# Optimization experiments

Hardware: AMD Instinct MI355X
Metric: run time of the kernel (lower is better)

The kernel has to match this reference:

```python
import jax, jax.numpy as jnp
import numpy as np

# irreps '32x0e + 32x1o + 16x2e': dims 32 (l=0), 96 (l=1, 32x3), 80 (l=2, 16x5) -> 208
MUL0, MUL1, MUL2 = 32, 32, 16
SC = 64  # scalar_channels
N_NODES, N_EDGES = 50000, 200000
FAN_IN = MUL0 * MUL0 + MUL1 * MUL1 + MUL2 * MUL2  # fully-connected path fan-in


def setup_inputs() -> dict:
    key = jax.random.key(0)
    ks = jax.random.split(key, 10)
    node_tensors = jax.random.normal(ks[0], (N_NODES, 208), dtype=jnp.float32)
    edge_index = jax.random.randint(ks[1], (2, N_EDGES), 0, N_NODES)
    # FullyConnectedTensorProduct path weights (mul1, mul2, mul_out)
    W0 = jax.random.normal(ks[2], (MUL0, MUL0, SC), dtype=jnp.float32)
    W1 = jax.random.normal(ks[3], (MUL1, MUL1, SC), dtype=jnp.float32)
    W2 = jax.random.normal(ks[4], (MUL2, MUL2, SC), dtype=jnp.float32)
    # MLP: Linear(64,32) -> SiLU -> Linear(32,1)
    A1 = jax.random.normal(ks[5], (SC, SC // 2), dtype=jnp.float32) / np.float32(np.sqrt(SC))
    b1 = jnp.zeros((SC // 2,), dtype=jnp.float32)
    A2 = jax.random.normal(ks[6], (SC // 2, 1), dtype=jnp.float32) / np.float32(np.sqrt(SC // 2))
    b2 = jnp.zeros((1,), dtype=jnp.float32)
    return {"node_tensors": node_tensors, "edge_index": edge_index,
            "W0": W0, "W1": W1, "W2": W2, "A1": A1, "b1": b1, "A2": A2, "b2": b2}


def _split_irreps(x):
    # x: [E, 208] -> scalars [E,32], vectors [E,32,3], rank-2 [E,16,5]
    s = x[:, :MUL0]
    v = x[:, MUL0:MUL0 + MUL1 * 3].reshape(-1, MUL1, 3)
    t = x[:, MUL0 + MUL1 * 3:].reshape(-1, MUL2, 5)
    return s, v, t


def reference(node_tensors, edge_index, W0, W1, W2, A1, b1, A2, b2):
    src, dst = edge_index[0], edge_index[1]
    x1 = node_tensors[src]  # [E, 208]
    x2 = node_tensors[dst]
    s1, v1, t1 = _split_irreps(x1)
    s2, v2, t2 = _split_irreps(x2)
    alpha = np.float32(1.0 / np.sqrt(FAN_IN))  # path normalization
    # l x l -> 0 Clebsch-Gordan: delta_{m1 m2} / sqrt(2l+1)
    e = alpha * (
        jnp.einsum('eu,ev,uvw->ew', s1, s2, W0)
        + jnp.einsum('eum,evm,uvw->ew', v1, v2, W1) / np.float32(np.sqrt(3.0))
        + jnp.einsum('eum,evm,uvw->ew', t1, t2, W2) / np.float32(np.sqrt(5.0))
    )  # [E, 64]
    h = jax.nn.silu(e @ A1 + b1)
    return (h @ A2 + b2)[:, 0]  # [E]
```

## Files before the change

### kernel.cpp

```cpp
#include <hip/hip_runtime.h>
#include <hip/hip_fp16.h>
#include <stdint.h>

#define N_EDGES 200000
#define N_NODES 50000
#define BM 32
#define NT 64

typedef _Float16 f16x8 __attribute__((ext_vector_type(8)));
typedef float f32x4 __attribute__((ext_vector_type(4)));

__global__ void prep_w(const float* __restrict__ W0, const float* __restrict__ W1,
                       const float* __restrict__ W2, uint16_t* __restrict__ wt) {
  int o = blockIdx.x * 256 + threadIdx.x;
  int T = o >> 11, r = o & 2047, w = r >> 5, kk = r & 31;
  int k = T * 32 + kk;
  const float AS = 1.0f / 48.0f;
  const float AV = AS * 0.57735026918962576f;
  const float AT = AS * 0.44721359549995794f;
  float val;
  if (k < 1024)      val = AS * W0[(k >> 5) * 2048 + (k & 31) * 64 + w];
  else if (k < 2048) { int k2 = k - 1024; val = AV * W1[(k2 >> 5) * 2048 + (k2 & 31) * 64 + w]; }
  else               { int k2 = k - 2048; val = AT * W2[(k2 >> 4) * 1024 + (k2 & 15) * 64 + w]; }
  __half h = __float2half(val);
  wt[o] = *reinterpret_cast<uint16_t*>(&h);
}

__global__ void prep_tables(const float* __restrict__ nt,
                            uint16_t* __restrict__ ta, uint16_t* __restrict__ tb) {
  long long o = (long long)blockIdx.x * 256 + threadIdx.x;
  if (o >= (long long)N_NODES * 296) return;
  int node = (int)(o / 296);
  int r = (int)(o - (long long)node * 296);
  const float* x = nt + (size_t)node * 208;
  float va = 0.f;
  if (r < 32) va = x[r];
  else if (r < 160) { int q = r - 32;  int u = q >> 2, m = q & 3;  if (m < 3) va = x[32 + u * 3 + m]; }
  else if (r < 288) { int q = r - 160; int u = q >> 3, m = q & 7;  if (m < 5) va = x[128 + u * 5 + m]; }
  __half ha = __float2half(va);
  ta[(size_t)node * 296 + r] = *reinterpret_cast<uint16_t*>(&ha);
  if (r < 216) {
    float vb = 0.f;
    if (r < 32) vb = x[r];
    else if (r < 128) { int q = r - 32;  int m = q >> 5, v = q & 31; vb = x[32 + v * 3 + m]; }
    else if (r < 208) { int q = r - 128; int m = q >> 4, v = q & 15; vb = x[128 + v * 5 + m]; }
    __half hb = __float2half(vb);
    tb[(size_t)node * 216 + r] = *reinterpret_cast<uint16_t*>(&hb);
  }
}

__device__ __forceinline__ void gload16(const void* g, void* l) {
  __builtin_amdgcn_global_load_lds(
      (const __attribute__((address_space(1))) void*)g,
      (__attribute__((address_space(3))) void*)l, 16, 0, 0);
}

#define LOADW(WRA, TEXPR)                                                       \
  { int Tc_ = (TEXPR);                                                          \
    _Pragma("unroll") for (int nf = 0; nf < 4; ++nf)                            \
      WRA[nf] = wtg4[Tc_ * 256 + nf * 64 + lo4]; }

#define MSTEPA(WRA, A)                                                          \
  _Pragma("unroll") for (int mf = 0; mf < 2; ++mf)                              \
  _Pragma("unroll") for (int nf = 0; nf < 4; ++nf)                              \
    acc[mf][nf] = __builtin_amdgcn_mfma_f32_16x16x32_f16(                       \
        (A)[mf], *(const f16x8*)&WRA[nf], acc[mf][nf], 0, 0, 0);

#define BUILD_S(T_, A)                                                          \
  _Pragma("unroll") for (int mf = 0; mf < 2; ++mf) {                            \
    __half s1v = *(const __half*)(x1b[mf] + 2 * (T_));                          \
    __half2 s1b2 = __half2half2(s1v);                                           \
    union { uint32_t u[4]; f16x8 v; } au_;                                      \
    _Pragma("unroll") for (int q = 0; q < 4; ++q) {                             \
      __half2 p = __hmul2(s1b2, ((const __half2*)&s2pk[mf])[q]);                \
      au_.u[q] = *(uint32_t*)&p;                                                \
    }                                                                           \
    (A)[mf] = au_.v;                                                            \
  }

#define BUILD_V(U_, A)                                                          \
  _Pragma("unroll") for (int mf = 0; mf < 2; ++mf) {                            \
    uint2 vv_ = *(const uint2*)(x1b[mf] + 64 + (U_) * 8);                       \
    __half2 h01_ = *(__half2*)&vv_.x;                                           \
    __half2 h2x_ = *(__half2*)&vv_.y;                                           \
    __half2 va0 = __half2half2(__low2half(h01_));                               \
    __half2 va1 = __half2half2(__high2half(h01_));                              \
    __half2 va2 = __half2half2(__low2half(h2x_));                               \
    union { uint32_t u[4]; f16x8 v; } au_;                                      \
    _Pragma("unroll") for (int q = 0; q < 4; ++q) {                             \
      __half2 p = __hmul2(va0, ((const __half2*)&v2pk[mf][0])[q]);              \
      p = __hfma2(va1, ((const __half2*)&v2pk[mf][1])[q], p);                   \
      p = __hfma2(va2, ((const __half2*)&v2pk[mf][2])[q], p);                   \
      au_.u[q] = *(uint32_t*)&p;                                                \
    }                                                                           \
    (A)[mf] = au_.v;                                                            \
  }

#define BUILD_T(TT_, A)                                                         \
  _Pragma("unroll") for (int mm = 0; mm < 2; ++mm) {                            \
    int u_ = (TT_) * 2 + (g >> 1);                                              \
    uint4 tv_ = *(const uint4*)(x1b[mm] + 320 + u_ * 16);                       \
    __half2 w01_ = *(__half2*)&tv_.x;                                           \
    __half2 w23_ = *(__half2*)&tv_.y;                                           \
    __half2 w4x_ = *(__half2*)&tv_.z;                                           \
    __half2 tb0 = __half2half2(__low2half(w01_));                               \
    __half2 tb1 = __half2half2(__high2half(w01_));                              \
    __half2 tb2 = __half2half2(__low2half(w23_));                               \
    __half2 tb3 = __half2half2(__high2half(w23_));                              \
    __half2 tb4 = __half2half2(__low2half(w4x_));                               \
    union { uint32_t u[4]; f16x8 v; } au_;                                      \
    _Pragma("unroll") for (int q = 0; q < 4; ++q) {                             \
      __half2 p = __hmul2(tb0, ((const __half2*)&t2pk[mm][0])[q]);              \
      p = __hfma2(tb1, ((const __half2*)&t2pk[mm][1])[q], p);                   \
      p = __hfma2(tb2, ((const __half2*)&t2pk[mm][2])[q], p);                   \
      p = __hfma2(tb3, ((const __half2*)&t2pk[mm][3])[q], p);                   \
      p = __hfma2(tb4, ((const __half2*)&t2pk[mm][4])[q], p);                   \
      au_.u[q] = *(uint32_t*)&p;                                                \
    }                                                                           \
    (A)[mm] = au_.v;                                                            \
  }

#define RING_S(WRA, P, T0) { f16x8 a[2]; BUILD_S((T0) + (P), a); MSTEPA(WRA, a); LOADW(WRA, (T0) + (P) + 4); }
#define RING_V(WRA, P, T0) { f16x8 a[2]; BUILD_V((T0) + (P) - 32, a); MSTEPA(WRA, a); LOADW(WRA, (T0) + (P) + 4); }
#define WRAPT(X) ((X) <= 71 ? (X) : (X) - 8)
#define RING_T(WRA, P, T0) { f16x8 a[2]; BUILD_T((T0) + (P) - 64, a); MSTEPA(WRA, a); LOADW(WRA, WRAPT((T0) + (P) + 4)); }

__global__ __launch_bounds__(NT) void edge_main(
    const uint16_t* __restrict__ ta, const uint16_t* __restrict__ tbl,
    const int* __restrict__ ei, const uint16_t* __restrict__ wt,
    const float* __restrict__ A1, const float* __restrict__ b1,
    const float* __restrict__ A2, const float* __restrict__ b2,
    float* __restrict__ out)
{
  __shared__ alignas(16) unsigned char smem[18944];
  const int tid = threadIdx.x;
  const int e0 = blockIdx.x * BM;

  {
    #pragma unroll
    for (int i = 0; i < 18; ++i) {
      unsigned idx = i * 64 + tid;
      unsigned row = idx / 37u;
      unsigned cj = idx - row * 37u;
      int e = e0 + (int)row;
      int src = ei[e];
      const char* gp = (const char*)ta + (size_t)src * 592 + cj * 16;
      gload16(gp, (void*)(smem + i * 1024));
    }
    if (tid < 32) {
      unsigned idx = 1152 + tid;
      unsigned row = idx / 37u;
      unsigned cj = idx - row * 37u;
      int e = e0 + (int)row;
      int src = ei[e];
      const char* gp = (const char*)ta + (size_t)src * 592 + cj * 16;
      gload16(gp, (void*)(smem + 18432));
    }
  }
  asm volatile("s_waitcnt vmcnt(0)" ::: "memory");

  const int lane = tid, c = lane & 15, g = lane >> 4;
  const int lo4 = c * 4 + g;

  const unsigned char* x1b[2];
  const unsigned char* tbp[2];
  #pragma unroll
  for (int mf = 0; mf < 2; ++mf) {
    int erow = mf * 16 + c;
    x1b[mf] = smem + (size_t)erow * 592;
    int e = e0 + erow;
    int dst = ei[N_EDGES + e];
    tbp[mf] = (const unsigned char*)tbl + (size_t)dst * 432;
  }

  f32x4 acc[2][4];
  #pragma unroll
  for (int mf = 0; mf < 2; ++mf)
    #pragma unroll
    for (int nf = 0; nf < 4; ++nf) acc[mf][nf] = (f32x4){0.f, 0.f, 0.f, 0.f};

  const uint4* wtg4 = (const uint4*)wt;
  uint4 wr0[4], wr1[4], wr2[4], wr3[4];

  {
    uint4 s2pk[2];
    #pragma unroll
    for (int mf = 0; mf < 2; ++mf) s2pk[mf] = *(const uint4*)(tbp[mf] + g * 16);
    LOADW(wr0, 0); LOADW(wr1, 1); LOADW(wr2, 2); LOADW(wr3, 3);
    for (int T = 0; T < 32; T += 4) {
      RING_S(wr0, 0, T); RING_S(wr1, 1, T); RING_S(wr2, 2, T); RING_S(wr3, 3, T);
    }
  }
  {
    uint4 v2pk[2][3];
    #pragma unroll
    for (int mf = 0; mf < 2; ++mf)
      #pragma unroll
      for (int m3 = 0; m3 < 3; ++m3)
        v2pk[mf][m3] = *(const uint4*)(tbp[mf] + 64 + m3 * 64 + g * 16);
    for (int T = 32; T < 64; T += 4) {
      RING_V(wr0, 0, T); RING_V(wr1, 1, T); RING_V(wr2, 2, T); RING_V(wr3, 3, T);
    }
  }
  {
    uint4 t2pk[2][5];
    #pragma unroll
    for (int mm = 0; mm < 2; ++mm)
      #pragma unroll
      for (int m5 = 0; m5 < 5; ++m5)
        t2pk[mm][m5] = *(const uint4*)(tbp[mm] + 256 + m5 * 32 + (g & 1) * 16);
    RING_T(wr0, 0, 64); RING_T(wr1, 1, 64); RING_T(wr2, 2, 64); RING_T(wr3, 3, 64);
    RING_T(wr0, 0, 68); RING_T(wr1, 1, 68); RING_T(wr2, 2, 68); RING_T(wr3, 3, 68);
  }

  float* ew = (float*)smem;
  #pragma unroll
  for (int mf = 0; mf < 2; ++mf)
    #pragma unroll
    for (int nf = 0; nf < 4; ++nf)
      #pragma unroll
      for (int rr = 0; rr < 4; ++rr)
        ew[(size_t)(mf * 16 + g * 4 + rr) * 68 + nf * 16 + c] = acc[mf][nf][rr];

  {
    int el = lane >> 1, jh = lane & 1;
    const float* er = ew + (size_t)el * 68;
    float hacc[16];
    #pragma unroll
    for (int j = 0; j < 16; ++j) hacc[j] = b1[jh * 16 + j];
    for (int w4 = 0; w4 < 16; ++w4) {
      float4 ea = *(const float4*)(er + w4 * 4);
      #pragma unroll
      for (int q2 = 0; q2 < 4; ++q2) {
        float ev = (&ea.x)[q2];
        int w = w4 * 4 + q2;
        float4 a0 = *(const float4*)(A1 + w * 32 + jh * 16);
        float4 a1 = *(const float4*)(A1 + w * 32 + jh * 16 + 4);
        float4 a2 = *(const float4*)(A1 + w * 32 + jh * 16 + 8);
        float4 a3 = *(const float4*)(A1 + w * 32 + jh * 16 + 12);
        hacc[0]  += ev * a0.x; hacc[1]  += ev * a0.y; hacc[2]  += ev * a0.z; hacc[3]  += ev * a0.w;
        hacc[4]  += ev * a1.x; hacc[5]  += ev * a1.y; hacc[6]  += ev * a1.z; hacc[7]  += ev * a1.w;
        hacc[8]  += ev * a2.x; hacc[9]  += ev * a2.y; hacc[10] += ev * a2.z; hacc[11] += ev * a2.w;
        hacc[12] += ev * a3.x; hacc[13] += ev * a3.y; hacc[14] += ev * a3.z; hacc[15] += ev * a3.w;
      }
    }
    float o = 0.f;
    #pragma unroll
    for (int j = 0; j < 16; ++j) {
      float z = hacc[j];
      o += (z / (1.f + __expf(-z))) * A2[jh * 16 + j];
    }
    o += __shfl_xor(o, 1);
    int e = e0 + el;
    if (jh == 0 && e < N_EDGES) out[e] = o + b2[0];
  }
}

extern "C" void kernel_launch(void* const* d_in, const int* in_sizes, int n_in,
                              void* d_out, int out_size, void* d_ws, size_t ws_size,
                              hipStream_t stream) {
  const float* nt = (const float*)d_in[0];
  const int*   ei = (const int*)d_in[1];
  const float* W0 = (const float*)d_in[2];
  const float* W1 = (const float*)d_in[3];
  const float* W2 = (const float*)d_in[4];
  const float* A1 = (const float*)d_in[5];
  const float* b1 = (const float*)d_in[6];
  const float* A2 = (const float*)d_in[7];
  const float* b2 = (const float*)d_in[8];
  float* out = (float*)d_out;

  uint16_t* wt = (uint16_t*)d_ws;
  uint16_t* ta = (uint16_t*)((char*)d_ws + 294912);
  uint16_t* tb = (uint16_t*)((char*)d_ws + 294912 + (size_t)N_NODES * 592);

  prep_w<<<576, 256, 0, stream>>>(W0, W1, W2, wt);
  {
    long long tot = (long long)N_NODES * 296;
    int blocks = (int)((tot + 255) / 256);
    prep_tables<<<blocks, 256, 0, stream>>>(nt, ta, tb);
  }
  edge_main<<<N_EDGES / BM, NT, 0, stream>>>(ta, tb, ei, wt, A1, b1, A2, b2, out);
}
```

Baseline: 221.0 us.

## Load source-node rows directly into registers instead of staging through LDS

Drops the global_load_lds staging of each edge's 32 source-node rows (about 19 KB of LDS) and the vmcnt(0) wait that came with it. Each lane now reads its own source row from global memory in 16-byte chunks into registers, and broadcasts halves with bit operations. LDS use shrinks to the small e-tile, so more blocks can be resident per CU. In exchange there are more scattered global loads inside the MFMA loop and more register pressure. A __syncthreads is added before the e-tile is read back.

```diff
diff --git a/kernel.cpp b/kernel.cpp
--- a/kernel.cpp
+++ b/kernel.cpp
@@ -49,10 +49,11 @@
   }
 }
 
-__device__ __forceinline__ void gload16(const void* g, void* l) {
-  __builtin_amdgcn_global_load_lds(
-      (const __attribute__((address_space(1))) void*)g,
-      (__attribute__((address_space(3))) void*)l, 16, 0, 0);
+__device__ __forceinline__ __half2 bcast_half(uint32_t w, int sel) {
+  uint32_t hv = sel ? (w >> 16) : (w & 0xffffu);
+  hv |= hv << 16;
+  union { uint32_t u; __half2 h; } cv; cv.u = hv;
+  return cv.h;
 }
 
 #define LOADW(WRA, TEXPR)                                                       \
@@ -66,10 +67,9 @@
     acc[mf][nf] = __builtin_amdgcn_mfma_f32_16x16x32_f16(                       \
         (A)[mf], *(const f16x8*)&WRA[nf], acc[mf][nf], 0, 0, 0);
 
-#define BUILD_S(T_, A)                                                          \
+#define BUILD_SR(T_, A)                                                         \
   _Pragma("unroll") for (int mf = 0; mf < 2; ++mf) {                            \
-    __half s1v = *(const __half*)(x1b[mf] + 2 * (T_));                          \
-    __half2 s1b2 = __half2half2(s1v);                                           \
+    __half2 s1b2 = bcast_half(sS[mf][(T_) >> 1], (T_) & 1);                     \
     union { uint32_t u[4]; f16x8 v; } au_;                                      \
     _Pragma("unroll") for (int q = 0; q < 4; ++q) {                             \
       __half2 p = __hmul2(s1b2, ((const __half2*)&s2pk[mf])[q]);                \
@@ -78,14 +78,11 @@
     (A)[mf] = au_.v;                                                            \
   }
 
-#define BUILD_V(U_, A)                                                          \
+#define BUILD_VR(UL, A)                                                         \
   _Pragma("unroll") for (int mf = 0; mf < 2; ++mf) {                            \
-    uint2 vv_ = *(const uint2*)(x1b[mf] + 64 + (U_) * 8);                       \
-    __half2 h01_ = *(__half2*)&vv_.x;                                           \
-    __half2 h2x_ = *(__half2*)&vv_.y;                                           \
-    __half2 va0 = __half2half2(__low2half(h01_));                               \
-    __half2 va1 = __half2half2(__high2half(h01_));                              \
-    __half2 va2 = __half2half2(__low2half(h2x_));                               \
+    __half2 va0 = bcast_half(vS[mf][(UL) * 2], 0);                              \
+    __half2 va1 = bcast_half(vS[mf][(UL) * 2], 1);                              \
+    __half2 va2 = bcast_half(vS[mf][(UL) * 2 + 1], 0);                          \
     union { uint32_t u[4]; f16x8 v; } au_;                                      \
     _Pragma("unroll") for (int q = 0; q < 4; ++q) {                             \
       __half2 p = __hmul2(va0, ((const __half2*)&v2pk[mf][0])[q]);              \
@@ -96,18 +93,13 @@
     (A)[mf] = au_.v;                                                            \
   }
 
-#define BUILD_T(TT_, A)                                                         \
+#define BUILD_TR(TT_, A)                                                        \
   _Pragma("unroll") for (int mm = 0; mm < 2; ++mm) {                            \
-    int u_ = (TT_) * 2 + (g >> 1);                                              \
-    uint4 tv_ = *(const uint4*)(x1b[mm] + 320 + u_ * 16);                       \
-    __half2 w01_ = *(__half2*)&tv_.x;                                           \
-    __half2 w23_ = *(__half2*)&tv_.y;                                           \
-    __half2 w4x_ = *(__half2*)&tv_.z;                                           \
-    __half2 tb0 = __half2half2(__low2half(w01_));                               \
-    __half2 tb1 = __half2half2(__high2half(w01_));                              \
-    __half2 tb2 = __half2half2(__low2half(w23_));                               \
-    __half2 tb3 = __half2half2(__high2half(w23_));                              \
-    __half2 tb4 = __half2half2(__low2half(w4x_));                               \
+    __half2 tb0 = bcast_half(tS[mm][(TT_) * 4 + 0], 0);                         \
+    __half2 tb1 = bcast_half(tS[mm][(TT_) * 4 + 0], 1);                         \
+    __half2 tb2 = bcast_half(tS[mm][(TT_) * 4 + 1], 0);                         \
+    __half2 tb3 = bcast_half(tS[mm][(TT_) * 4 + 1], 1);                         \
+    __half2 tb4 = bcast_half(tS[mm][(TT_) * 4 + 2], 0);                         \
     union { uint32_t u[4]; f16x8 v; } au_;                                      \
     _Pragma("unroll") for (int q = 0; q < 4; ++q) {                             \
       __half2 p = __hmul2(tb0, ((const __half2*)&t2pk[mm][0])[q]);              \
@@ -120,10 +112,10 @@
     (A)[mm] = au_.v;                                                            \
   }
 
-#define RING_S(WRA, P, T0) { f16x8 a[2]; BUILD_S((T0) + (P), a); MSTEPA(WRA, a); LOADW(WRA, (T0) + (P) + 4); }
-#define RING_V(WRA, P, T0) { f16x8 a[2]; BUILD_V((T0) + (P) - 32, a); MSTEPA(WRA, a); LOADW(WRA, (T0) + (P) + 4); }
+#define RING_SR(WRA, T_)     { f16x8 a[2]; BUILD_SR(T_, a); MSTEPA(WRA, a); LOADW(WRA, (T_) + 4); }
+#define RING_VR(WRA, UL, TB) { f16x8 a[2]; BUILD_VR(UL, a); MSTEPA(WRA, a); LOADW(WRA, (TB) + (UL) + 4); }
 #define WRAPT(X) ((X) <= 71 ? (X) : (X) - 8)
-#define RING_T(WRA, P, T0) { f16x8 a[2]; BUILD_T((T0) + (P) - 64, a); MSTEPA(WRA, a); LOADW(WRA, WRAPT((T0) + (P) + 4)); }
+#define RING_TR(WRA, TT_, TB){ f16x8 a[2]; BUILD_TR(TT_, a); MSTEPA(WRA, a); LOADW(WRA, WRAPT((TB) + (TT_) + 4)); }
 
 __global__ __launch_bounds__(NT) void edge_main(
     const uint16_t* __restrict__ ta, const uint16_t* __restrict__ tbl,
@@ -132,44 +124,20 @@
     const float* __restrict__ A2, const float* __restrict__ b2,
     float* __restrict__ out)
 {
-  __shared__ alignas(16) unsigned char smem[18944];
+  __shared__ alignas(16) float etile[32 * 68];
   const int tid = threadIdx.x;
   const int e0 = blockIdx.x * BM;
-
-  {
-    #pragma unroll
-    for (int i = 0; i < 18; ++i) {
-      unsigned idx = i * 64 + tid;
-      unsigned row = idx / 37u;
-      unsigned cj = idx - row * 37u;
-      int e = e0 + (int)row;
-      int src = ei[e];
-      const char* gp = (const char*)ta + (size_t)src * 592 + cj * 16;
-      gload16(gp, (void*)(smem + i * 1024));
-    }
-    if (tid < 32) {
-      unsigned idx = 1152 + tid;
-      unsigned row = idx / 37u;
-      unsigned cj = idx - row * 37u;
-      int e = e0 + (int)row;
-      int src = ei[e];
-      const char* gp = (const char*)ta + (size_t)src * 592 + cj * 16;
-      gload16(gp, (void*)(smem + 18432));
-    }
-  }
-  asm volatile("s_waitcnt vmcnt(0)" ::: "memory");
-
   const int lane = tid, c = lane & 15, g = lane >> 4;
   const int lo4 = c * 4 + g;
 
-  const unsigned char* x1b[2];
+  const unsigned char* x1p[2];
   const unsigned char* tbp[2];
   #pragma unroll
   for (int mf = 0; mf < 2; ++mf) {
-    int erow = mf * 16 + c;
-    x1b[mf] = smem + (size_t)erow * 592;
-    int e = e0 + erow;
+    int e = e0 + mf * 16 + c;
+    int src = ei[e];
     int dst = ei[N_EDGES + e];
+    x1p[mf] = (const unsigned char*)ta + (size_t)src * 592;
     tbp[mf] = (const unsigned char*)tbl + (size_t)dst * 432;
   }
 
@@ -181,16 +149,28 @@
 
   const uint4* wtg4 = (const uint4*)wt;
   uint4 wr0[4], wr1[4], wr2[4], wr3[4];
+  LOADW(wr0, 0); LOADW(wr1, 1); LOADW(wr2, 2); LOADW(wr3, 3);
 
   {
     uint4 s2pk[2];
     #pragma unroll
     for (int mf = 0; mf < 2; ++mf) s2pk[mf] = *(const uint4*)(tbp[mf] + g * 16);
-    LOADW(wr0, 0); LOADW(wr1, 1); LOADW(wr2, 2); LOADW(wr3, 3);
-    for (int T = 0; T < 32; T += 4) {
-      RING_S(wr0, 0, T); RING_S(wr1, 1, T); RING_S(wr2, 2, T); RING_S(wr3, 3, T);
-    }
-  }
+    uint32_t sS[2][16];
+    #pragma unroll
+    for (int mf = 0; mf < 2; ++mf)
+      #pragma unroll
+      for (int i = 0; i < 4; ++i) {
+        uint4 q_ = *(const uint4*)(x1p[mf] + i * 16);
+        sS[mf][i * 4 + 0] = q_.x; sS[mf][i * 4 + 1] = q_.y;
+        sS[mf][i * 4 + 2] = q_.z; sS[mf][i * 4 + 3] = q_.w;
+      }
+    #pragma unroll
+    for (int T4 = 0; T4 < 8; ++T4) {
+      RING_SR(wr0, T4 * 4 + 0); RING_SR(wr1, T4 * 4 + 1);
+      RING_SR(wr2, T4 * 4 + 2); RING_SR(wr3, T4 * 4 + 3);
+    }
+  }
+
   {
     uint4 v2pk[2][3];
     #pragma unroll
@@ -198,10 +178,22 @@
       #pragma unroll
       for (int m3 = 0; m3 < 3; ++m3)
         v2pk[mf][m3] = *(const uint4*)(tbp[mf] + 64 + m3 * 64 + g * 16);
-    for (int T = 32; T < 64; T += 4) {
-      RING_V(wr0, 0, T); RING_V(wr1, 1, T); RING_V(wr2, 2, T); RING_V(wr3, 3, T);
-    }
-  }
+    for (int G = 0; G < 4; ++G) {
+      uint32_t vS[2][16];
+      #pragma unroll
+      for (int mf = 0; mf < 2; ++mf)
+        #pragma unroll
+        for (int i = 0; i < 4; ++i) {
+          uint4 q_ = *(const uint4*)(x1p[mf] + 64 + G * 64 + i * 16);
+          vS[mf][i * 4 + 0] = q_.x; vS[mf][i * 4 + 1] = q_.y;
+          vS[mf][i * 4 + 2] = q_.z; vS[mf][i * 4 + 3] = q_.w;
+        }
+      const int Tb = 32 + G * 8;
+      RING_VR(wr0, 0, Tb); RING_VR(wr1, 1, Tb); RING_VR(wr2, 2, Tb); RING_VR(wr3, 3, Tb);
+      RING_VR(wr0, 4, Tb); RING_VR(wr1, 5, Tb); RING_VR(wr2, 6, Tb); RING_VR(wr3, 7, Tb);
+    }
+  }
+
   {
     uint4 t2pk[2][5];
     #pragma unroll
@@ -209,22 +201,35 @@
       #pragma unroll
       for (int m5 = 0; m5 < 5; ++m5)
         t2pk[mm][m5] = *(const uint4*)(tbp[mm] + 256 + m5 * 32 + (g & 1) * 16);
-    RING_T(wr0, 0, 64); RING_T(wr1, 1, 64); RING_T(wr2, 2, 64); RING_T(wr3, 3, 64);
-    RING_T(wr0, 0, 68); RING_T(wr1, 1, 68); RING_T(wr2, 2, 68); RING_T(wr3, 3, 68);
-  }
-
-  float* ew = (float*)smem;
+    const int gh16 = (g >> 1) * 16;
+    #pragma unroll
+    for (int H = 0; H < 2; ++H) {
+      uint32_t tS[2][16];
+      #pragma unroll
+      for (int mm = 0; mm < 2; ++mm)
+        #pragma unroll
+        for (int i = 0; i < 4; ++i) {
+          uint4 q_ = *(const uint4*)(x1p[mm] + 320 + gh16 + H * 128 + i * 32);
+          tS[mm][i * 4 + 0] = q_.x; tS[mm][i * 4 + 1] = q_.y;
+          tS[mm][i * 4 + 2] = q_.z; tS[mm][i * 4 + 3] = q_.w;
+        }
+      const int Tb = 64 + H * 4;
+      RING_TR(wr0, 0, Tb); RING_TR(wr1, 1, Tb); RING_TR(wr2, 2, Tb); RING_TR(wr3, 3, Tb);
+    }
+  }
+
   #pragma unroll
   for (int mf = 0; mf < 2; ++mf)
     #pragma unroll
     for (int nf = 0; nf < 4; ++nf)
       #pragma unroll
       for (int rr = 0; rr < 4; ++rr)
-        ew[(size_t)(mf * 16 + g * 4 + rr) * 68 + nf * 16 + c] = acc[mf][nf][rr];
+        etile[(mf * 16 + g * 4 + rr) * 68 + nf * 16 + c] = acc[mf][nf][rr];
+  __syncthreads();
 
   {
     int el = lane >> 1, jh = lane & 1;
-    const float* er = ew + (size_t)el * 68;
+    const float* er = etile + (size_t)el * 68;
     float hacc[16];
     #pragma unroll
     for (int j = 0; j < 16; ++j) hacc[j] = b1[jh * 16 + j];
```

New measurement: 226.6 us. 2.6% more time.
